# Kernel tuning notes

Measured on AMD Instinct MI355X. Metric: run time of the kernel, lower is better.

## Reference

```python
import jax, jax.numpy as jnp
import numpy as np

N = 50000
E = 800000
IN_F, HID, OUT_F = 512, 256, 64
BN_EPS = 1e-5


def setup_inputs() -> dict:
    key = jax.random.key(0)
    ks = jax.random.split(key, 8)
    x = jax.random.normal(ks[0], (N, IN_F), dtype=jnp.float32)
    edge_rows = jax.random.randint(ks[1], (E,), 0, N, dtype=jnp.int32)
    edge_cols = jax.random.randint(ks[2], (E,), 0, N, dtype=jnp.int32)
    edge_vals = jax.random.uniform(ks[3], (E,), dtype=jnp.float32)
    # xavier_uniform for weights, zeros for biases (as in the torch module)
    lim1 = float(np.sqrt(6.0 / (IN_F + HID)))
    lim2 = float(np.sqrt(6.0 / (HID + OUT_F)))
    W1 = jax.random.uniform(ks[4], (IN_F, HID), minval=-lim1, maxval=lim1, dtype=jnp.float32)
    b1 = jnp.zeros((HID,), dtype=jnp.float32)
    W2 = jax.random.uniform(ks[5], (HID, OUT_F), minval=-lim2, maxval=lim2, dtype=jnp.float32)
    b2 = jnp.zeros((OUT_F,), dtype=jnp.float32)
    # BatchNorm affine params (torch defaults: weight=1, bias=0)
    gamma1 = jnp.ones((HID,), dtype=jnp.float32)
    beta1 = jnp.zeros((HID,), dtype=jnp.float32)
    gamma2 = jnp.ones((OUT_F,), dtype=jnp.float32)
    beta2 = jnp.zeros((OUT_F,), dtype=jnp.float32)
    return dict(x=x, edge_rows=edge_rows, edge_cols=edge_cols, edge_vals=edge_vals,
                W1=W1, b1=b1, gamma1=gamma1, beta1=beta1,
                W2=W2, b2=b2, gamma2=gamma2, beta2=beta2)


def _spmm(rows, cols, vals, dense):
    # sparse [N,N] @ dense [N,F] via gather + segment-sum scatter
    msgs = vals[:, None] * dense[cols]            # [E, F]
    return jax.ops.segment_sum(msgs, rows, num_segments=N)


def _batchnorm(h, gamma, beta):
    # training-mode BatchNorm1d: batch statistics over nodes (biased var)
    mean = jnp.mean(h, axis=0)
    var = jnp.var(h, axis=0)
    return gamma * (h - mean) * jax.lax.rsqrt(var + BN_EPS) + beta


def reference(x, edge_rows, edge_cols, edge_vals,
              W1, b1, gamma1, beta1, W2, b2, gamma2, beta2):
    # layer 1: GCN conv -> BN -> ReLU (dropout is identity in eval / reference)
    h = _spmm(edge_rows, edge_cols, edge_vals, x @ W1) + b1
    h = jax.nn.relu(_batchnorm(h, gamma1, beta1))
    # layer 2: GCN conv -> BN -> log_softmax over classes
    h = _spmm(edge_rows, edge_cols, edge_vals, h @ W2) + b2
    h = _batchnorm(h, gamma2, beta2)
    return jax.nn.log_softmax(h, axis=1)
```

## Files before the change

### kernel.cpp

```cpp
#include <hip/hip_runtime.h>

typedef __attribute__((ext_vector_type(8))) short short8;
typedef __attribute__((ext_vector_type(4))) float f32x4;
typedef __attribute__((ext_vector_type(8))) unsigned short ushort8;

__device__ __forceinline__ unsigned short f2bf(float f) {
  unsigned int u = __builtin_bit_cast(unsigned int, f);
  u += 0x7fffu + ((u >> 16) & 1u);
  return (unsigned short)(u >> 16);
}
__device__ __forceinline__ float bf2f(unsigned short b) {
  return __builtin_bit_cast(float, ((unsigned int)b) << 16);
}
__device__ __forceinline__ void gload_lds16(const void* g, void* l) {
  __builtin_amdgcn_global_load_lds(
      (const __attribute__((address_space(1))) void*)g,
      (__attribute__((address_space(3))) void*)l, 16, 0, 0);
}

__global__ __launch_bounds__(256) void cvt_weights(
    const float* __restrict__ W1, const float* __restrict__ W2,
    unsigned short* __restrict__ w1t, unsigned short* __restrict__ w2t)
{
  int idx = blockIdx.x * 256 + threadIdx.x;
  if (idx < 131072) {
    int n = idx >> 9, k = idx & 511;
    w1t[idx] = f2bf(W1[(size_t)k * 256 + n]);
  } else if (idx < 131072 + 16384) {
    int i = idx - 131072;
    int n = i >> 8, k = i & 255;
    w2t[i] = f2bf(W2[(size_t)k * 64 + n]);
  }
}

__global__ __launch_bounds__(256) void gemm1_mfma(
    const float* __restrict__ x,
    const unsigned short* __restrict__ w1t,
    unsigned short* __restrict__ H1,
    int M)
{
  __shared__ unsigned short As[2][64 * 32];
  __shared__ unsigned short Bs[2][256 * 32];
  const int tid = threadIdx.x;
  const int wid = tid >> 6, lane = tid & 63;
  const int wc = wid;
  const int m0 = blockIdx.x * 64;

  const int ar = tid >> 2;
  const int ac = tid & 3;
  const int arow = min(m0 + ar, M - 1);
  const int aphys = ac ^ ((ar >> 1) & 3);

  const int bq = lane >> 2;
  const int bslotx = (lane & 3) ^ ((lane >> 3) & 3);

  float4 alo, ahi;
  auto loadA = [&](int k0) {
    alo = *(const float4*)&x[(size_t)arow * 512 + k0 + ac * 8];
    ahi = *(const float4*)&x[(size_t)arow * 512 + k0 + ac * 8 + 4];
  };
  auto writeA = [&](int buf) {
    ushort8 o;
    o[0] = f2bf(alo.x); o[1] = f2bf(alo.y); o[2] = f2bf(alo.z); o[3] = f2bf(alo.w);
    o[4] = f2bf(ahi.x); o[5] = f2bf(ahi.y); o[6] = f2bf(ahi.z); o[7] = f2bf(ahi.w);
    *(ushort8*)((char*)As[buf] + ar * 64 + aphys * 16) = o;
  };
  auto stageB = [&](int k0, int buf) {
#pragma unroll
    for (int i = 0; i < 4; ++i) {
      int g = wid + 4 * i;
      int col = g * 16 + bq;
      gload_lds16(&w1t[(size_t)col * 512 + k0 + bslotx * 8],
                  (char*)Bs[buf] + g * 1024);
    }
  };

  f32x4 acc[4][4] = {};

  loadA(0);
  stageB(0, 0);
  writeA(0);
  __syncthreads();

  for (int kt = 0; kt < 16; ++kt) {
    const int cur = kt & 1, nxt = cur ^ 1;
    if (kt < 15) {
      loadA((kt + 1) * 32);
      stageB((kt + 1) * 32, nxt);
      asm volatile("s_waitcnt vmcnt(6)" ::: "memory");
    } else {
      asm volatile("s_waitcnt vmcnt(0)" ::: "memory");
    }
    short8 a[4], b[4];
#pragma unroll
    for (int m = 0; m < 4; ++m) {
      int row = m * 16 + (lane & 15);
      int phys = (lane >> 4) ^ ((row >> 1) & 3);
      a[m] = *(const short8*)((const char*)As[cur] + row * 64 + phys * 16);
    }
#pragma unroll
    for (int n = 0; n < 4; ++n) {
      int col = wc * 64 + n * 16 + (lane & 15);
      int phys = (lane >> 4) ^ ((col >> 1) & 3);
      b[n] = *(const short8*)((const char*)Bs[cur] + col * 64 + phys * 16);
    }
#pragma unroll
    for (int m = 0; m < 4; ++m)
#pragma unroll
      for (int n = 0; n < 4; ++n)
        acc[m][n] = __builtin_amdgcn_mfma_f32_16x16x32_bf16(a[m], b[n], acc[m][n], 0, 0, 0);
    if (kt < 15) writeA(nxt);
    asm volatile("s_waitcnt lgkmcnt(0)" ::: "memory");
    __builtin_amdgcn_s_barrier();
  }

  const int colbase = wc * 64 + (lane & 15);
#pragma unroll
  for (int m = 0; m < 4; ++m) {
    int rowbase = m0 + m * 16 + (lane >> 4) * 4;
#pragma unroll
    for (int j = 0; j < 4; ++j) {
      int row = rowbase + j;
      if (row < M) {
#pragma unroll
        for (int n = 0; n < 4; ++n)
          H1[(size_t)row * 256 + colbase + n * 16] = f2bf(acc[m][n][j]);
      }
    }
  }
}

__global__ __launch_bounds__(256) void gemm2_mfma(
    const unsigned short* __restrict__ A,
    const unsigned short* __restrict__ w2t,
    const float* __restrict__ scsh,
    unsigned short* __restrict__ H2,
    int M)
{
  __shared__ unsigned short As[128 * 64];
  __shared__ unsigned short Bs[64 * 64];
  const int tid = threadIdx.x;
  const int wid = tid >> 6, lane = tid & 63;
  const int wr = wid >> 1, wc = wid & 1;
  const int m0 = blockIdx.x * 128;

  const int srow = tid >> 3;
  const int ls = ((tid & 7) ^ (srow & 7)) * 8;
  const unsigned short* gB = &w2t[(size_t)srow * 256 + ls];
  char* lB = (char*)Bs + (size_t)wid * 1024;

  f32x4 acc[4][2] = {};

  for (int kt = 0; kt < 4; ++kt) {
    const int k0 = kt * 64;
#pragma unroll
    for (int i = 0; i < 2; ++i)
      gload_lds16(gB + (size_t)i * 32 * 256 + k0, lB + (size_t)i * 4096);
#pragma unroll
    for (int i = 0; i < 4; ++i) {
      int chunk = tid + 256 * i;
      int r = chunk >> 3, c = chunk & 7;
      int gk = k0 + c * 8;
      ushort8 u = *(const ushort8*)&A[(size_t)(m0 + r) * 256 + gk];
      float4 sc0 = *(const float4*)&scsh[gk];
      float4 sc1 = *(const float4*)&scsh[gk + 4];
      float4 sh0 = *(const float4*)&scsh[256 + gk];
      float4 sh1 = *(const float4*)&scsh[256 + gk + 4];
      ushort8 o;
      o[0] = f2bf(fmaxf(bf2f(u[0]) * sc0.x + sh0.x, 0.f));
      o[1] = f2bf(fmaxf(bf2f(u[1]) * sc0.y + sh0.y, 0.f));
      o[2] = f2bf(fmaxf(bf2f(u[2]) * sc0.z + sh0.z, 0.f));
      o[3] = f2bf(fmaxf(bf2f(u[3]) * sc0.w + sh0.w, 0.f));
      o[4] = f2bf(fmaxf(bf2f(u[4]) * sc1.x + sh1.x, 0.f));
      o[5] = f2bf(fmaxf(bf2f(u[5]) * sc1.y + sh1.y, 0.f));
      o[6] = f2bf(fmaxf(bf2f(u[6]) * sc1.z + sh1.z, 0.f));
      o[7] = f2bf(fmaxf(bf2f(u[7]) * sc1.w + sh1.w, 0.f));
      *(ushort8*)((char*)As + r * 128 + ((c ^ (r & 7)) * 16)) = o;
    }
    __syncthreads();

#pragma unroll
    for (int kk = 0; kk < 2; ++kk) {
      short8 a[4], b[2];
#pragma unroll
      for (int m = 0; m < 4; ++m) {
        int row = wr * 64 + m * 16 + (lane & 15);
        int phys = (kk * 4 + (lane >> 4)) ^ (row & 7);
        a[m] = *(const short8*)((const char*)As + row * 128 + phys * 16);
      }
#pragma unroll
      for (int n = 0; n < 2; ++n) {
        int col = wc * 32 + n * 16 + (lane & 15);
        int phys = (kk * 4 + (lane >> 4)) ^ (col & 7);
        b[n] = *(const short8*)((const char*)Bs + col * 128 + phys * 16);
      }
#pragma unroll
      for (int m = 0; m < 4; ++m)
#pragma unroll
        for (int n = 0; n < 2; ++n)
          acc[m][n] = __builtin_amdgcn_mfma_f32_16x16x32_bf16(a[m], b[n], acc[m][n], 0, 0, 0);
    }
    __syncthreads();
  }

  const int colbase = wc * 32 + (lane & 15);
#pragma unroll
  for (int m = 0; m < 4; ++m) {
    int rowbase = m0 + wr * 64 + m * 16 + (lane >> 4) * 4;
#pragma unroll
    for (int j = 0; j < 4; ++j) {
      int row = rowbase + j;
      if (row < M) {
#pragma unroll
        for (int n = 0; n < 2; ++n)
          H2[(size_t)row * 64 + colbase + n * 16] = f2bf(acc[m][n][j]);
      }
    }
  }
}

__global__ __launch_bounds__(256) void edge_hist(
    const int* __restrict__ rows, int* __restrict__ cnt, int E)
{
  int e = blockIdx.x * 256 + threadIdx.x;
  if (e < E) atomicAdd(&cnt[rows[e]], 1);
}

__global__ __launch_bounds__(256) void scan_blocksum(
    const int* __restrict__ cnt, int* __restrict__ bsum, int Nrows)
{
  int i = blockIdx.x * 256 + threadIdx.x;
  int v = (i < Nrows) ? cnt[i] : 0;
#pragma unroll
  for (int off = 1; off < 64; off <<= 1) v += __shfl_xor(v, off);
  __shared__ int wsum[4];
  if ((threadIdx.x & 63) == 0) wsum[threadIdx.x >> 6] = v;
  __syncthreads();
  if (threadIdx.x == 0)
    bsum[blockIdx.x] = wsum[0] + wsum[1] + wsum[2] + wsum[3];
}

__global__ __launch_bounds__(256) void scan_boff(
    const int* __restrict__ bsum, int* __restrict__ boff, int NB)
{
  __shared__ int lds[256];
  int t = threadIdx.x;
  int v = (t < NB) ? bsum[t] : 0;
  lds[t] = v;
  __syncthreads();
  for (int off = 1; off < 256; off <<= 1) {
    int u = (t >= off) ? lds[t - off] : 0;
    __syncthreads();
    lds[t] += u;
    __syncthreads();
  }
  boff[t] = (t == 0) ? 0 : lds[t - 1];
}

__global__ __launch_bounds__(256) void scan_write(
    const int* __restrict__ cnt, const int* __restrict__ boff,
    int* __restrict__ rowptr, int* __restrict__ cursor, int Nrows, int E)
{
  __shared__ int lds[256];
  int t = threadIdx.x;
  int i = blockIdx.x * 256 + t;
  int v = (i < Nrows) ? cnt[i] : 0;
  lds[t] = v;
  __syncthreads();
  for (int off = 1; off < 256; off <<= 1) {
    int u = (t >= off) ? lds[t - off] : 0;
    __syncthreads();
    lds[t] += u;
    __syncthreads();
  }
  int excl = boff[blockIdx.x] + lds[t] - v;
  if (i < Nrows) { rowptr[i] = excl; cursor[i] = excl; }
  if (i == Nrows) rowptr[i] = E;
}

__global__ __launch_bounds__(256) void edge_scatter(
    const int* __restrict__ rows, const int* __restrict__ cols,
    const float* __restrict__ vals, int* __restrict__ cursor,
    int2* __restrict__ spack, int E)
{
  int e = blockIdx.x * 256 + threadIdx.x;
  if (e < E) {
    int r = rows[e];
    int p = atomicAdd(&cursor[r], 1);
    spack[p] = make_int2(cols[e], __float_as_int(vals[e]));
  }
}

__global__ __launch_bounds__(256) void spmm_gather_bf(
    const int* __restrict__ rowptr, const int2* __restrict__ sp,
    const unsigned short* __restrict__ D,
    unsigned short* __restrict__ out, int Nrows)
{
  const int lane = threadIdx.x & 63;
  const int r = blockIdx.x * 4 + (threadIdx.x >> 6);
  if (r >= Nrows) return;
  const int s = rowptr[r], e = rowptr[r + 1];
  float4 acc0 = make_float4(0.f, 0.f, 0.f, 0.f);
  float4 acc1 = make_float4(0.f, 0.f, 0.f, 0.f);
  int j = s;
  for (; j + 7 < e; j += 8) {
    int2 p[8];
    ushort4 d[8];
#pragma unroll
    for (int t = 0; t < 8; ++t) p[t] = sp[j + t];
#pragma unroll
    for (int t = 0; t < 8; ++t)
      d[t] = *(const ushort4*)&D[(size_t)p[t].x * 256 + lane * 4];
#pragma unroll
    for (int t = 0; t < 8; t += 2) {
      float v0 = __int_as_float(p[t].y), v1 = __int_as_float(p[t + 1].y);
      acc0.x = fmaf(v0, bf2f(d[t].x), acc0.x); acc0.y = fmaf(v0, bf2f(d[t].y), acc0.y);
      acc0.z = fmaf(v0, bf2f(d[t].z), acc0.z); acc0.w = fmaf(v0, bf2f(d[t].w), acc0.w);
      acc1.x = fmaf(v1, bf2f(d[t + 1].x), acc1.x); acc1.y = fmaf(v1, bf2f(d[t + 1].y), acc1.y);
      acc1.z = fmaf(v1, bf2f(d[t + 1].z), acc1.z); acc1.w = fmaf(v1, bf2f(d[t + 1].w), acc1.w);
    }
  }
  for (; j + 1 < e; j += 2) {
    int2 p0 = sp[j], p1 = sp[j + 1];
    ushort4 d0 = *(const ushort4*)&D[(size_t)p0.x * 256 + lane * 4];
    ushort4 d1 = *(const ushort4*)&D[(size_t)p1.x * 256 + lane * 4];
    float v0 = __int_as_float(p0.y), v1 = __int_as_float(p1.y);
    acc0.x = fmaf(v0, bf2f(d0.x), acc0.x); acc0.y = fmaf(v0, bf2f(d0.y), acc0.y);
    acc0.z = fmaf(v0, bf2f(d0.z), acc0.z); acc0.w = fmaf(v0, bf2f(d0.w), acc0.w);
    acc1.x = fmaf(v1, bf2f(d1.x), acc1.x); acc1.y = fmaf(v1, bf2f(d1.y), acc1.y);
    acc1.z = fmaf(v1, bf2f(d1.z), acc1.z); acc1.w = fmaf(v1, bf2f(d1.w), acc1.w);
  }
  if (j < e) {
    int2 p = sp[j];
    float v = __int_as_float(p.y);
    ushort4 d = *(const ushort4*)&D[(size_t)p.x * 256 + lane * 4];
    acc0.x = fmaf(v, bf2f(d.x), acc0.x); acc0.y = fmaf(v, bf2f(d.y), acc0.y);
    acc0.z = fmaf(v, bf2f(d.z), acc0.z); acc0.w = fmaf(v, bf2f(d.w), acc0.w);
  }
  ushort4 ov;
  ov.x = f2bf(acc0.x + acc1.x); ov.y = f2bf(acc0.y + acc1.y);
  ov.z = f2bf(acc0.z + acc1.z); ov.w = f2bf(acc0.w + acc1.w);
  *(ushort4*)&out[(size_t)r * 256 + lane * 4] = ov;
}

__global__ __launch_bounds__(256) void spmm_gather_bf64(
    const int* __restrict__ rowptr, const int2* __restrict__ sp,
    const unsigned short* __restrict__ D,
    float* __restrict__ out, int Nrows)
{
  const int lane = threadIdx.x & 63;
  const int r = blockIdx.x * 4 + (threadIdx.x >> 6);
  if (r >= Nrows) return;
  const int s = rowptr[r], e = rowptr[r + 1];
  float acc0 = 0.f, acc1 = 0.f;
  int j = s;
  for (; j + 7 < e; j += 8) {
    int2 p[8];
    float d[8];
#pragma unroll
    for (int t = 0; t < 8; ++t) p[t] = sp[j + t];
#pragma unroll
    for (int t = 0; t < 8; ++t) d[t] = bf2f(D[(size_t)p[t].x * 64 + lane]);
#pragma unroll
    for (int t = 0; t < 8; t += 2) {
      acc0 = fmaf(__int_as_float(p[t].y), d[t], acc0);
      acc1 = fmaf(__int_as_float(p[t + 1].y), d[t + 1], acc1);
    }
  }
  for (; j < e; ++j) {
    int2 p = sp[j];
    acc0 = fmaf(__int_as_float(p.y), bf2f(D[(size_t)p.x * 64 + lane]), acc0);
  }
  out[(size_t)r * 64 + lane] = acc0 + acc1;
}

__global__ __launch_bounds__(256) void bn_stats_bf256(
    const unsigned short* __restrict__ H, float* __restrict__ partials, int Nrows)
{
  const int cc = threadIdx.x & 31;
  const int c = cc * 8;
  const int rr = threadIdx.x >> 5;
  float s[8] = {}, q[8] = {};
  for (int r = blockIdx.x * 8 + rr; r < Nrows; r += gridDim.x * 8) {
    ushort8 u = *(const ushort8*)&H[(size_t)r * 256 + c];
#pragma unroll
    for (int j = 0; j < 8; ++j) {
      float f = bf2f(u[j]);
      s[j] += f; q[j] += f * f;
    }
  }
  __shared__ float lds[256][16];
  float* L = lds[threadIdx.x];
#pragma unroll
  for (int j = 0; j < 8; ++j) { L[j] = s[j]; L[8 + j] = q[j]; }
  __syncthreads();
  if (rr == 0) {
#pragma unroll
    for (int r2 = 1; r2 < 8; ++r2) {
      float* Mm = lds[cc + r2 * 32];
#pragma unroll
      for (int j = 0; j < 8; ++j) { s[j] += Mm[j]; q[j] += Mm[8 + j]; }
    }
    float* P = &partials[(size_t)blockIdx.x * 512];
#pragma unroll
    for (int j = 0; j < 8; ++j) { P[c + j] = s[j]; P[256 + c + j] = q[j]; }
  }
}

__global__ __launch_bounds__(256) void bn_stats64(
    const float* __restrict__ H, float* __restrict__ partials, int Nrows)
{
  const int cc = threadIdx.x % 16;
  const int c = cc * 4;
  const int rr = threadIdx.x / 16;
  float4 s = make_float4(0.f, 0.f, 0.f, 0.f);
  float4 q = make_float4(0.f, 0.f, 0.f, 0.f);
  for (int r = blockIdx.x * 16 + rr; r < Nrows; r += gridDim.x * 16) {
    float4 v = *(const float4*)&H[(size_t)r * 64 + c];
    s.x += v.x; s.y += v.y; s.z += v.z; s.w += v.w;
    q.x += v.x * v.x; q.y += v.y * v.y; q.z += v.z * v.z; q.w += v.w * v.w;
  }
  __shared__ float lds[256][8];
  float* L = lds[threadIdx.x];
  L[0] = s.x; L[1] = s.y; L[2] = s.z; L[3] = s.w;
  L[4] = q.x; L[5] = q.y; L[6] = q.z; L[7] = q.w;
  __syncthreads();
  if (rr == 0) {
#pragma unroll
    for (int r2 = 1; r2 < 16; ++r2) {
      float* Mm = lds[cc + r2 * 16];
      s.x += Mm[0]; s.y += Mm[1]; s.z += Mm[2]; s.w += Mm[3];
      q.x += Mm[4]; q.y += Mm[5]; q.z += Mm[6]; q.w += Mm[7];
    }
    float* P = &partials[(size_t)blockIdx.x * 128];
    *(float4*)&P[c] = s;
    *(float4*)&P[64 + c] = q;
  }
}

template<int C>
__global__ __launch_bounds__(256) void bn_finalize_par(
    const float* __restrict__ partials,
    const float* __restrict__ gamma, const float* __restrict__ beta,
    float* __restrict__ scsh, int G, float invN)
{
  const int c = blockIdx.x;
  const int t = threadIdx.x;
  float sum = 0.f, sq = 0.f;
  for (int g = t; g < G; g += 256) {
    sum += partials[(size_t)g * 2 * C + c];
    sq  += partials[(size_t)g * 2 * C + C + c];
  }
#pragma unroll
  for (int off = 1; off < 64; off <<= 1) {
    sum += __shfl_xor(sum, off);
    sq  += __shfl_xor(sq, off);
  }
  __shared__ float ws[4][2];
  if ((t & 63) == 0) { ws[t >> 6][0] = sum; ws[t >> 6][1] = sq; }
  __syncthreads();
  if (t == 0) {
    sum = ws[0][0] + ws[1][0] + ws[2][0] + ws[3][0];
    sq  = ws[0][1] + ws[1][1] + ws[2][1] + ws[3][1];
    float mean = sum * invN;
    float var = sq * invN - mean * mean;
    float rstd = rsqrtf(var + 1e-5f);
    float sc = gamma[c] * rstd;
    scsh[c] = sc;
    scsh[C + c] = beta[c] - mean * sc;
  }
}

__global__ __launch_bounds__(256) void bn_lsm(
    const float* __restrict__ H, const float* __restrict__ scsh,
    float* __restrict__ out, int Nrows)
{
  int lane = threadIdx.x & 63;
  int r = blockIdx.x * 4 + (threadIdx.x >> 6);
  if (r >= Nrows) return;
  float y = H[(size_t)r * 64 + lane] * scsh[lane] + scsh[64 + lane];
  float m = y;
#pragma unroll
  for (int off = 32; off >= 1; off >>= 1) m = fmaxf(m, __shfl_xor(m, off));
  float ex = expf(y - m);
  float s = ex;
#pragma unroll
  for (int off = 32; off >= 1; off >>= 1) s += __shfl_xor(s, off);
  out[(size_t)r * 64 + lane] = (y - m) - logf(s);
}

extern "C" void kernel_launch(void* const* d_in, const int* in_sizes, int n_in,
                              void* d_out, int out_size, void* d_ws, size_t ws_size,
                              hipStream_t stream) {
  const float* x      = (const float*)d_in[0];
  const int*   erow   = (const int*)  d_in[1];
  const int*   ecol   = (const int*)  d_in[2];
  const float* eval   = (const float*)d_in[3];
  const float* W1     = (const float*)d_in[4];
  const float* gamma1 = (const float*)d_in[6];
  const float* beta1  = (const float*)d_in[7];
  const float* W2     = (const float*)d_in[8];
  const float* gamma2 = (const float*)d_in[10];
  const float* beta2  = (const float*)d_in[11];

  const int N = in_sizes[0] / 512;
  const int E = in_sizes[1];

  char* ws = (char*)d_ws;
  unsigned short* H1b   = (unsigned short*)(ws + 0);
  float* partials1      = (float*)(ws + 0);
  unsigned short* H2b   = (unsigned short*)(ws + 0);
  float* H2AGG          = (float*)(ws + 12800000);
  unsigned short* H1AGGb= (unsigned short*)(ws + 51200000);
  float* partials2      = (float*)(ws + 51200000);
  unsigned short* w1t   = (unsigned short*)(ws + 76865536);
  float* scsh1          = (float*)(ws + 77127680);
  float* scsh2          = (float*)(ws + 77129728);
  int*   rowptr         = (int*)(ws + 77130240);
  int*   cnt            = (int*)(ws + 77330244);
  int*   cursor         = (int*)(ws + 77530244);
  int2*  spack          = (int2*)(ws + 77730248);
  int*   bsum           = (int*)(ws + 84130248);
  int*   boff           = (int*)(ws + 84131272);
  unsigned short* w2t   = (unsigned short*)(ws + 84132352);

  hipMemsetAsync(cnt, 0, (size_t)N * 4, stream);

  const dim3 blk(256);
  const int eblocks = (E + 255) / 256;
  const int NB = (N + 255) / 256;

  edge_hist<<<eblocks, blk, 0, stream>>>(erow, cnt, E);
  scan_blocksum<<<NB, blk, 0, stream>>>(cnt, bsum, N);
  scan_boff<<<1, blk, 0, stream>>>(bsum, boff, NB);
  scan_write<<<NB + 1, blk, 0, stream>>>(cnt, boff, rowptr, cursor, N, E);
  edge_scatter<<<eblocks, blk, 0, stream>>>(erow, ecol, eval, cursor, spack, E);

  cvt_weights<<<576, blk, 0, stream>>>(W1, W2, w1t, w2t);

  gemm1_mfma<<<(N + 63) / 64, blk, 0, stream>>>(x, w1t, H1b, N);
  spmm_gather_bf<<<(N + 3) / 4, blk, 0, stream>>>(rowptr, spack, H1b, H1AGGb, N);
  bn_stats_bf256<<<256, blk, 0, stream>>>(H1AGGb, partials1, N);
  bn_finalize_par<256><<<256, blk, 0, stream>>>(partials1, gamma1, beta1, scsh1, 256, 1.0f / N);
  gemm2_mfma<<<(N + 127) / 128, blk, 0, stream>>>(H1AGGb, w2t, scsh1, H2b, N);
  spmm_gather_bf64<<<(N + 3) / 4, blk, 0, stream>>>(rowptr, spack, H2b, H2AGG, N);
  bn_stats64<<<256, blk, 0, stream>>>(H2AGG, partials2, N);
  bn_finalize_par<64><<<64, blk, 0, stream>>>(partials2, gamma2, beta2, scsh2, 256, 1.0f / N);
  bn_lsm<<<(N + 3) / 4, blk, 0, stream>>>(H2AGG, scsh2, (float*)d_out, N);
}
```

Before: 280.0 us.

## Fuse weight conversion with histogram, GEMM1 with edge scatter, SpMM2 with BN stats

Merges independent kernels into shared launches. Weight conversion now shares a grid with the edge histogram, and the CSR edge scatter is appended as extra blocks of the first GEMM. The second SpMM also writes per-block BN partial sums, which removes the separate stats pass over H2AGG. The GEMM loop's hand-tuned vmcnt waits are replaced by a plain __syncthreads, which may weaken load/compute overlap. The BN finalize now reduces many more partials (G2 ≈ 12500 instead of 256), and the partials2 buffer grows accordingly, so it may overlap other workspace regions.

```diff
diff --git a/kernel.cpp b/kernel.cpp
--- a/kernel.cpp
+++ b/kernel.cpp
@@ -18,29 +18,50 @@
       (__attribute__((address_space(3))) void*)l, 16, 0, 0);
 }
 
-__global__ __launch_bounds__(256) void cvt_weights(
+__global__ __launch_bounds__(256) void cvt_and_hist(
     const float* __restrict__ W1, const float* __restrict__ W2,
-    unsigned short* __restrict__ w1t, unsigned short* __restrict__ w2t)
-{
-  int idx = blockIdx.x * 256 + threadIdx.x;
-  if (idx < 131072) {
-    int n = idx >> 9, k = idx & 511;
-    w1t[idx] = f2bf(W1[(size_t)k * 256 + n]);
-  } else if (idx < 131072 + 16384) {
-    int i = idx - 131072;
-    int n = i >> 8, k = i & 255;
-    w2t[i] = f2bf(W2[(size_t)k * 64 + n]);
-  }
-}
-
-__global__ __launch_bounds__(256) void gemm1_mfma(
+    unsigned short* __restrict__ w1t, unsigned short* __restrict__ w2t,
+    const int* __restrict__ rows, int* __restrict__ cnt, int E)
+{
+  int b = blockIdx.x;
+  if (b < 576) {
+    int idx = b * 256 + threadIdx.x;
+    if (idx < 131072) {
+      int n = idx >> 9, k = idx & 511;
+      w1t[idx] = f2bf(W1[(size_t)k * 256 + n]);
+    } else if (idx < 131072 + 16384) {
+      int i = idx - 131072;
+      int n = i >> 8, k = i & 255;
+      w2t[i] = f2bf(W2[(size_t)k * 64 + n]);
+    }
+  } else {
+    int e = (b - 576) * 256 + threadIdx.x;
+    if (e < E) atomicAdd(&cnt[rows[e]], 1);
+  }
+}
+
+__global__ __launch_bounds__(256) void gemm1_scatter(
     const float* __restrict__ x,
     const unsigned short* __restrict__ w1t,
     unsigned short* __restrict__ H1,
-    int M)
+    int M, int G1,
+    const int* __restrict__ erow, const int* __restrict__ ecol,
+    const float* __restrict__ eval, int* __restrict__ cursor,
+    int2* __restrict__ spack, int E)
 {
   __shared__ unsigned short As[2][64 * 32];
   __shared__ unsigned short Bs[2][256 * 32];
+
+  if ((int)blockIdx.x >= G1) {
+    int e = ((int)blockIdx.x - G1) * 256 + threadIdx.x;
+    if (e < E) {
+      int r = erow[e];
+      int p = atomicAdd(&cursor[r], 1);
+      spack[p] = make_int2(ecol[e], __float_as_int(eval[e]));
+    }
+    return;
+  }
+
   const int tid = threadIdx.x;
   const int wid = tid >> 6, lane = tid & 63;
   const int wc = wid;
@@ -87,9 +108,6 @@
     if (kt < 15) {
       loadA((kt + 1) * 32);
       stageB((kt + 1) * 32, nxt);
-      asm volatile("s_waitcnt vmcnt(6)" ::: "memory");
-    } else {
-      asm volatile("s_waitcnt vmcnt(0)" ::: "memory");
     }
     short8 a[4], b[4];
 #pragma unroll
@@ -110,8 +128,7 @@
       for (int n = 0; n < 4; ++n)
         acc[m][n] = __builtin_amdgcn_mfma_f32_16x16x32_bf16(a[m], b[n], acc[m][n], 0, 0, 0);
     if (kt < 15) writeA(nxt);
-    asm volatile("s_waitcnt lgkmcnt(0)" ::: "memory");
-    __builtin_amdgcn_s_barrier();
+    __syncthreads();
   }
 
   const int colbase = wc * 64 + (lane & 15);
@@ -219,13 +236,6 @@
   }
 }
 
-__global__ __launch_bounds__(256) void edge_hist(
-    const int* __restrict__ rows, int* __restrict__ cnt, int E)
-{
-  int e = blockIdx.x * 256 + threadIdx.x;
-  if (e < E) atomicAdd(&cnt[rows[e]], 1);
-}
-
 __global__ __launch_bounds__(256) void scan_blocksum(
     const int* __restrict__ cnt, int* __restrict__ bsum, int Nrows)
 {
@@ -276,19 +286,6 @@
   int excl = boff[blockIdx.x] + lds[t] - v;
   if (i < Nrows) { rowptr[i] = excl; cursor[i] = excl; }
   if (i == Nrows) rowptr[i] = E;
-}
-
-__global__ __launch_bounds__(256) void edge_scatter(
-    const int* __restrict__ rows, const int* __restrict__ cols,
-    const float* __restrict__ vals, int* __restrict__ cursor,
-    int2* __restrict__ spack, int E)
-{
-  int e = blockIdx.x * 256 + threadIdx.x;
-  if (e < E) {
-    int r = rows[e];
-    int p = atomicAdd(&cursor[r], 1);
-    spack[p] = make_int2(cols[e], __float_as_int(vals[e]));
-  }
 }
 
 __global__ __launch_bounds__(256) void spmm_gather_bf(
@@ -343,35 +340,49 @@
   *(ushort4*)&out[(size_t)r * 256 + lane * 4] = ov;
 }
 
-__global__ __launch_bounds__(256) void spmm_gather_bf64(
+__global__ __launch_bounds__(256) void spmm2_stats(
     const int* __restrict__ rowptr, const int2* __restrict__ sp,
     const unsigned short* __restrict__ D,
-    float* __restrict__ out, int Nrows)
+    float* __restrict__ out, float* __restrict__ partials, int Nrows)
 {
   const int lane = threadIdx.x & 63;
-  const int r = blockIdx.x * 4 + (threadIdx.x >> 6);
-  if (r >= Nrows) return;
-  const int s = rowptr[r], e = rowptr[r + 1];
+  const int w = threadIdx.x >> 6;
+  const int r = blockIdx.x * 4 + w;
   float acc0 = 0.f, acc1 = 0.f;
-  int j = s;
-  for (; j + 7 < e; j += 8) {
-    int2 p[8];
-    float d[8];
-#pragma unroll
-    for (int t = 0; t < 8; ++t) p[t] = sp[j + t];
-#pragma unroll
-    for (int t = 0; t < 8; ++t) d[t] = bf2f(D[(size_t)p[t].x * 64 + lane]);
-#pragma unroll
-    for (int t = 0; t < 8; t += 2) {
-      acc0 = fmaf(__int_as_float(p[t].y), d[t], acc0);
-      acc1 = fmaf(__int_as_float(p[t + 1].y), d[t + 1], acc1);
-    }
-  }
-  for (; j < e; ++j) {
-    int2 p = sp[j];
-    acc0 = fmaf(__int_as_float(p.y), bf2f(D[(size_t)p.x * 64 + lane]), acc0);
-  }
-  out[(size_t)r * 64 + lane] = acc0 + acc1;
+  if (r < Nrows) {
+    const int s = rowptr[r], e = rowptr[r + 1];
+    int j = s;
+    for (; j + 7 < e; j += 8) {
+      int2 p[8];
+      float d[8];
+#pragma unroll
+      for (int t = 0; t < 8; ++t) p[t] = sp[j + t];
+#pragma unroll
+      for (int t = 0; t < 8; ++t) d[t] = bf2f(D[(size_t)p[t].x * 64 + lane]);
+#pragma unroll
+      for (int t = 0; t < 8; t += 2) {
+        acc0 = fmaf(__int_as_float(p[t].y), d[t], acc0);
+        acc1 = fmaf(__int_as_float(p[t + 1].y), d[t + 1], acc1);
+      }
+    }
+    for (; j < e; ++j) {
+      int2 p = sp[j];
+      acc0 = fmaf(__int_as_float(p.y), bf2f(D[(size_t)p.x * 64 + lane]), acc0);
+    }
+  }
+  float val = acc0 + acc1;
+  if (r < Nrows) out[(size_t)r * 64 + lane] = val;
+  if (r >= Nrows) val = 0.f;
+  __shared__ float ls[4][128];
+  ls[w][lane] = val;
+  ls[w][64 + lane] = val * val;
+  __syncthreads();
+  if (w == 0) {
+    float s2 = ls[0][lane] + ls[1][lane] + ls[2][lane] + ls[3][lane];
+    float q2 = ls[0][64 + lane] + ls[1][64 + lane] + ls[2][64 + lane] + ls[3][64 + lane];
+    partials[(size_t)blockIdx.x * 128 + lane] = s2;
+    partials[(size_t)blockIdx.x * 128 + 64 + lane] = q2;
+  }
 }
 
 __global__ __launch_bounds__(256) void bn_stats_bf256(
@@ -404,37 +415,6 @@
     float* P = &partials[(size_t)blockIdx.x * 512];
 #pragma unroll
     for (int j = 0; j < 8; ++j) { P[c + j] = s[j]; P[256 + c + j] = q[j]; }
-  }
-}
-
-__global__ __launch_bounds__(256) void bn_stats64(
-    const float* __restrict__ H, float* __restrict__ partials, int Nrows)
-{
-  const int cc = threadIdx.x % 16;
-  const int c = cc * 4;
-  const int rr = threadIdx.x / 16;
-  float4 s = make_float4(0.f, 0.f, 0.f, 0.f);
-  float4 q = make_float4(0.f, 0.f, 0.f, 0.f);
-  for (int r = blockIdx.x * 16 + rr; r < Nrows; r += gridDim.x * 16) {
-    float4 v = *(const float4*)&H[(size_t)r * 64 + c];
-    s.x += v.x; s.y += v.y; s.z += v.z; s.w += v.w;
-    q.x += v.x * v.x; q.y += v.y * v.y; q.z += v.z * v.z; q.w += v.w * v.w;
-  }
-  __shared__ float lds[256][8];
-  float* L = lds[threadIdx.x];
-  L[0] = s.x; L[1] = s.y; L[2] = s.z; L[3] = s.w;
-  L[4] = q.x; L[5] = q.y; L[6] = q.z; L[7] = q.w;
-  __syncthreads();
-  if (rr == 0) {
-#pragma unroll
-    for (int r2 = 1; r2 < 16; ++r2) {
-      float* Mm = lds[cc + r2 * 16];
-      s.x += Mm[0]; s.y += Mm[1]; s.z += Mm[2]; s.w += Mm[3];
-      q.x += Mm[4]; q.y += Mm[5]; q.z += Mm[6]; q.w += Mm[7];
-    }
-    float* P = &partials[(size_t)blockIdx.x * 128];
-    *(float4*)&P[c] = s;
-    *(float4*)&P[64 + c] = q;
   }
 }
 
@@ -529,22 +509,20 @@
   const dim3 blk(256);
   const int eblocks = (E + 255) / 256;
   const int NB = (N + 255) / 256;
-
-  edge_hist<<<eblocks, blk, 0, stream>>>(erow, cnt, E);
+  const int G1 = (N + 63) / 64;
+
+  cvt_and_hist<<<576 + eblocks, blk, 0, stream>>>(W1, W2, w1t, w2t, erow, cnt, E);
   scan_blocksum<<<NB, blk, 0, stream>>>(cnt, bsum, N);
   scan_boff<<<1, blk, 0, stream>>>(bsum, boff, NB);
   scan_write<<<NB + 1, blk, 0, stream>>>(cnt, boff, rowptr, cursor, N, E);
-  edge_scatter<<<eblocks, blk, 0, stream>>>(erow, ecol, eval, cursor, spack, E);
-
-  cvt_weights<<<576, blk, 0, stream>>>(W1, W2, w1t, w2t);
-
-  gemm1_mfma<<<(N + 63) / 64, blk, 0, stream>>>(x, w1t, H1b, N);
+  gemm1_scatter<<<G1 + eblocks, blk, 0, stream>>>(
+      x, w1t, H1b, N, G1, erow, ecol, eval, cursor, spack, E);
   spmm_gather_bf<<<(N + 3) / 4, blk, 0, stream>>>(rowptr, spack, H1b, H1AGGb, N);
   bn_stats_bf256<<<256, blk, 0, stream>>>(H1AGGb, partials1, N);
   bn_finalize_par<256><<<256, blk, 0, stream>>>(partials1, gamma1, beta1, scsh1, 256, 1.0f / N);
   gemm2_mfma<<<(N + 127) / 128, blk, 0, stream>>>(H1AGGb, w2t, scsh1, H2b, N);
-  spmm_gather_bf64<<<(N + 3) / 4, blk, 0, stream>>>(rowptr, spack, H2b, H2AGG, N);
-  bn_stats64<<<256, blk, 0, stream>>>(H2AGG, partials2, N);
-  bn_finalize_par<64><<<64, blk, 0, stream>>>(partials2, gamma2, beta2, scsh2, 256, 1.0f / N);
+  const int G2 = (N + 3) / 4;
+  spmm2_stats<<<G2, blk, 0, stream>>>(rowptr, spack, H2b, H2AGG, partials2, N);
+  bn_finalize_par<64><<<64, blk, 0, stream>>>(partials2, gamma2, beta2, scsh2, G2, 1.0f / N);
   bn_lsm<<<(N + 3) / 4, blk, 0, stream>>>(H2AGG, scsh2, (float*)d_out, N);
 }
```

After: 298.3 us. 1.07x slower.
